# Kernel tuning notes

Hardware: AMD Instinct MI355X
Metric: run time of the kernel (lower is better)

## Reference

```python
import jax, jax.numpy as jnp
import numpy as np

# ---- constants from the source module ----
NB = [[0,1,2,3],[0,1,4],[0,2,5],[0,3,6],[1,4,7],[2,5,8],[3,6,9],[4,7,10],[5,8,11],[6,9],[7,10],[8,11],[12,13,14,15],[12,13,16],[12,14,17],[12,15],[13,16,18],[14,17,19],[16,18,20],[17,19,21],[18,20,22],[19,21,23],[20,22],[21,23]]
PARENT = np.array([0,0,0,0,1,2,3,4,5,6,7,8,9,9,9,12,13,14,16,17,18,19,20,21])  # root parent sentinel handled separately
KJ, NV, PREG = 24, 6890, 200
LEN = np.array([len(n) for n in NB])
NBR_IDX = np.zeros((KJ,4), np.int32)
NBR_VALID = np.zeros((KJ,4), np.float32)
for k, n in enumerate(NB):
    NBR_IDX[k,:len(n)] = n; NBR_VALID[k,:len(n)] = 1.0
BETA_POS = np.zeros((KJ,17), np.float32); BETA_POS[np.arange(KJ), 4*LEN] = 1.0
SLICE_MASK = np.zeros((23,17), np.float32)
for j in range(23):
    SLICE_MASK[j,:4*LEN[j]+1] = 1.0  # self.K[j] has 4*len(NB[j])+1 rows
NBR_IDX = jnp.asarray(NBR_IDX); NBR_VALID = jnp.asarray(NBR_VALID)
BETA_POS = jnp.asarray(BETA_POS); SLICE_MASK = jnpp = jnp.asarray(SLICE_MASK)


def setup_inputs() -> dict:
    key = jax.random.key(0)
    ks = jax.random.split(key, 9)
    V = jax.random.normal(ks[0], (PREG, NV, 3), jnp.float32)
    T = jax.random.normal(ks[1], (PREG, NV, 3), jnp.float32)
    J = jax.random.normal(ks[2], (PREG, KJ, 3), jnp.float32)
    theta = 0.3 * jax.random.normal(ks[3], (PREG, 72), jnp.float32)
    W_prime = jax.random.uniform(ks[4], (NV, KJ), jnp.float32)
    W_i = jax.random.uniform(ks[5], (NV, KJ), jnp.float32)
    W_i = W_i / W_i.sum(axis=1, keepdims=True)
    A = jax.random.uniform(ks[6], (23, NV), jnp.float32)
    K_mats = 0.01 * jax.random.normal(ks[7], (23, 17, 3 * NV), jnp.float32)
    K_mats = K_mats * SLICE_MASK[:, :, None]  # zero rows beyond the ragged per-joint size
    beta_2 = jnp.ones((1,), jnp.float32)
    return {"V": V, "T": T, "J": J, "theta": theta, "W_prime": W_prime, "W_i": W_i, "A": A, "K_mats": K_mats, "beta_2": beta_2, "epoch": 1}


def _rodrigues(pose):  # pose: (K,3)
    angle = jnp.maximum(jnp.linalg.norm(pose, axis=1, keepdims=True), 1e-8)
    axis = pose / angle
    x, y, z = axis[:, 0], axis[:, 1], axis[:, 2]
    zero = jnp.zeros_like(x)
    skew = jnp.stack([zero, -z, y, z, zero, -x, -y, x, zero], axis=1).reshape(-1, 3, 3)
    outer = axis[:, :, None] * axis[:, None, :]
    c = jnp.cos(angle)[:, :, None]
    s = jnp.sin(angle)[:, :, None]
    eye = jnp.eye(3, dtype=pose.dtype)[None]
    return c * eye + (1.0 - c) * outer + s * skew


def _compute_G(pose72, Jp):  # pose72: (72,), Jp: (K,3) -> (K,4,4)
    R = _rodrigues(pose72.reshape(KJ, 3))
    t = Jp - jnp.concatenate([jnp.zeros((1, 3), Jp.dtype), Jp[PARENT[1:]]], axis=0)
    G_local = jnp.zeros((KJ, 4, 4), Jp.dtype)
    G_local = G_local.at[:, :3, :3].set(R).at[:, :3, 3].set(t).at[:, 3, 3].set(1.0)
    Gs = [G_local[0]]
    for i in range(1, KJ):  # fixed 24-joint kinematic tree
        Gs.append(Gs[PARENT[i]] @ G_local[i])
    G = jnp.stack(Gs, axis=0)
    off = jnp.einsum('kij,kj->ki', G[:, :3, :3], Jp)  # homogeneous w=0 -> rotation only
    return G.at[:, :3, 3].add(-off)


def _axis2quat(p):  # (M,3) -> (M,4)
    angle = jnp.sqrt(jnp.maximum(jnp.sum(p ** 2, axis=1), 1e-16))
    n = p / angle[:, None]
    s = jnp.sin(angle / 2)
    return jnp.stack([n[:, 0] * s, n[:, 1] * s, n[:, 2] * s, jnp.cos(angle / 2) - 1.0], axis=1)


def reference(V, T, J, theta, W_prime, W_i, A, K_mats, beta_2, epoch):
    P = V.shape[0]
    b2 = beta_2[0]
    # normalized skinning weights
    W_relu = jax.nn.relu(W_prime)
    W_change = W_relu / (W_relu.sum(axis=1, keepdims=True) + 1e-8)
    # per-pose global joint transforms
    G_prime = jax.vmap(_compute_G)(theta, J)  # (P,K,4,4)
    # quaternion features and blend-shape correction
    q = _axis2quat(theta.reshape(P * KJ, 3)).reshape(P, KJ, 4)
    qg = q[:, NBR_IDX, :] * NBR_VALID[None, :, :, None]       # (P,K,4,4) neighbor gather
    q17 = jnp.concatenate([qg.reshape(P, KJ, 16), jnp.zeros((P, KJ, 1), q.dtype)], axis=-1)
    q17 = q17 + BETA_POS[None] * b2                            # beta_2 at column 4*len
    qm = q17[:, 1:, :] * SLICE_MASK[None]                      # ragged slice q_ne[:, j+1, :lenK]
    contrib = jnp.einsum('pjl,jlm->pjm', qm, K_mats).reshape(P, 23, NV, 3)
    T_p = jnp.einsum('pjnc,jn->pnc', contrib, jax.nn.relu(A)) + T
    # linear blend skinning
    T_h = jnp.concatenate([T_p, jnp.ones((P, NV, 1), T_p.dtype)], axis=-1)
    transformed = jnp.einsum('pkij,pnj->pnki', G_prime[:, :, :3, :], T_h)  # (P,N,K,3)
    verts = jnp.einsum('nk,pnkc->pnc', W_change, transformed)
    # energies
    e = float(epoch)
    g_wi = 0.1 * np.exp(-0.1 * e)
    g_w = 0.002 * np.exp(-0.008 * e)
    g_a = 0.001 * np.exp(-0.008 * e)
    g_k = 0.1 * np.exp(-0.008 * e)
    E_D = jnp.sum((V - verts) ** 2)
    E_Wi = jnp.sum((W_change - W_i) ** 2)
    E_W = jnp.sum(jnp.abs(W_change))
    E_A = jnp.sum(jnp.abs(A))
    E_K = jnp.sum(jnp.sqrt(jnp.sum(K_mats ** 2, axis=(1, 2))))
    E = E_D + g_wi * E_Wi + g_w * E_W + g_a * E_A + g_k * E_K
    return (E, verts)
```

## Files before the change

kernel.cpp:

```cpp
#include <hip/hip_runtime.h>
#include <math.h>

#define KJ 24
#define NV 6890
#define PREG 200
#define M_TOT (NV*3)
#define KDIM 391
#define KPAD 416
#define TP_STRIDE 20672
#define NMTILE 323

#define EDP_OFF 0
#define EKP_OFF 2816
#define WIP_OFF 10248
#define EWP_OFF 10280
#define EAP_OFF 10312
#define RED_OFF 10344
#define G_OFF   10384
#define WT_OFF  67984
#define RA_OFF  233344
#define QBH_OFF_U 1417600
#define QBL_OFF_U 1524096
#define TP_OFF  815296

typedef __attribute__((ext_vector_type(8))) short short8;
typedef __attribute__((ext_vector_type(4))) float f32x4;

__constant__ int c_PARENT[24] = {0,0,0,0,1,2,3,4,5,6,7,8,9,9,9,12,13,14,16,17,18,19,20,21};
__constant__ int c_DEPTH[24]  = {0,1,1,1,2,2,2,3,3,3,4,4,4,4,4,5,5,5,6,6,7,7,8,8};
__constant__ int c_LEN[24]    = {4,3,3,3,3,3,3,3,3,2,2,2,4,3,3,2,3,3,3,3,3,3,2,2};
__constant__ int c_NBR[24][4] = {
  {0,1,2,3},{0,1,4,0},{0,2,5,0},{0,3,6,0},{1,4,7,0},{2,5,8,0},{3,6,9,0},{4,7,10,0},
  {5,8,11,0},{6,9,0,0},{7,10,0,0},{8,11,0,0},{12,13,14,15},{12,13,16,0},{12,14,17,0},
  {12,15,0,0},{13,16,18,0},{14,17,19,0},{16,18,20,0},{17,19,21,0},{18,20,22,0},
  {19,21,23,0},{20,22,0,0},{21,23,0,0}};

__device__ __forceinline__ float waveReduce(float v) {
  #pragma unroll
  for (int off = 32; off > 0; off >>= 1) v += __shfl_down(v, off, 64);
  return v;
}
__device__ __forceinline__ unsigned short f2bf(float x) {
  union { float f; unsigned u; } v; v.f = x;
  unsigned r = v.u + 0x7FFFu + ((v.u >> 16) & 1u);
  return (unsigned short)(r >> 16);
}
__device__ __forceinline__ float bf2f(unsigned short h) {
  union { unsigned u; float f; } v; v.u = ((unsigned)h) << 16; return v.f;
}

__global__ __launch_bounds__(256) void kPre(const float* __restrict__ J,
                                            const float* __restrict__ theta,
                                            const float* __restrict__ beta2,
                                            const float* __restrict__ Wp,
                                            const float* __restrict__ Wi,
                                            const float* __restrict__ A,
                                            float* __restrict__ ws) {
  unsigned short* qbh = (unsigned short*)ws + QBH_OFF_U;
  unsigned short* qbl = (unsigned short*)ws + QBL_OFF_U;
  int b = blockIdx.x;
  if (b < 50) {
    __shared__ float Gl[4][24][12];
    __shared__ float Gg[4][24][12];
    __shared__ float q[4][24][4];
    int w = threadIdx.x >> 6, t = threadIdx.x & 63;
    int p = b*4 + w;
    if (t < 24) {
      float x = theta[p*72 + 3*t + 0];
      float y = theta[p*72 + 3*t + 1];
      float z = theta[p*72 + 3*t + 2];
      float n2 = x*x + y*y + z*z;
      float ang = fmaxf(sqrtf(n2), 1e-8f);
      float ia = 1.f/ang;
      float ax = x*ia, ay = y*ia, az = z*ia;
      float c = cosf(ang), s = sinf(ang), C = 1.f - c;
      float jx = J[p*72+3*t], jy = J[p*72+3*t+1], jz = J[p*72+3*t+2];
      float tx = jx, ty = jy, tz = jz;
      if (t > 0) {
        int par = c_PARENT[t];
        tx -= J[p*72+3*par]; ty -= J[p*72+3*par+1]; tz -= J[p*72+3*par+2];
      }
      Gl[w][t][0]=c+C*ax*ax;   Gl[w][t][1]=C*ax*ay-s*az; Gl[w][t][2]=C*ax*az+s*ay; Gl[w][t][3]=tx;
      Gl[w][t][4]=C*ax*ay+s*az;Gl[w][t][5]=c+C*ay*ay;    Gl[w][t][6]=C*ay*az-s*ax; Gl[w][t][7]=ty;
      Gl[w][t][8]=C*ax*az-s*ay;Gl[w][t][9]=C*ay*az+s*ax; Gl[w][t][10]=c+C*az*az;   Gl[w][t][11]=tz;
      float ang2 = sqrtf(fmaxf(n2, 1e-16f));
      float inv2 = 1.f/ang2;
      float s2 = sinf(0.5f*ang2);
      q[w][t][0] = x*inv2*s2; q[w][t][1] = y*inv2*s2; q[w][t][2] = z*inv2*s2;
      q[w][t][3] = cosf(0.5f*ang2) - 1.f;
    }
    __syncthreads();
    for (int lev = 0; lev <= 8; lev++) {
      if (t < 24 && c_DEPTH[t] == lev) {
        if (lev == 0) {
          for (int i2 = 0; i2 < 12; i2++) Gg[w][0][i2] = Gl[w][0][i2];
        } else {
          int par = c_PARENT[t];
          for (int r = 0; r < 3; r++) {
            float g0 = Gg[w][par][r*4+0], g1 = Gg[w][par][r*4+1];
            float g2 = Gg[w][par][r*4+2], g3 = Gg[w][par][r*4+3];
            for (int c2 = 0; c2 < 4; c2++) {
              float v = g0*Gl[w][t][0+c2] + g1*Gl[w][t][4+c2] + g2*Gl[w][t][8+c2];
              if (c2 == 3) v += g3;
              Gg[w][t][r*4+c2] = v;
            }
          }
        }
      }
      __syncthreads();
    }
    if (t < 24) {
      float jx = J[p*72+3*t], jy = J[p*72+3*t+1], jz = J[p*72+3*t+2];
      float* gp = ws + G_OFF + p*288 + t*12;
      #pragma unroll
      for (int r = 0; r < 3; r++) {
        float off = Gg[w][t][r*4+0]*jx + Gg[w][t][r*4+1]*jy + Gg[w][t][r*4+2]*jz;
        Gg[w][t][r*4+3] -= off;
      }
      #pragma unroll
      for (int i2 = 0; i2 < 12; i2++) gp[i2] = Gg[w][t][i2];
    }
    __syncthreads();
    float b2 = beta2[0];
    for (int e = t; e < KDIM; e += 64) {
      int j = e / 17, l = e - 17*j;
      int k = j + 1;
      float val = 0.f;
      if (l < 4*c_LEN[j] + 1) {
        if (l < 16) {
          int sidx = l >> 2, cc = l & 3;
          if (sidx < c_LEN[k]) val = q[w][c_NBR[k][sidx]][cc];
        }
        if (l == 4*c_LEN[k]) val += b2;
      }
      unsigned short hi = f2bf(val);
      unsigned short lo = f2bf(val - bf2f(hi));
      qbh[p*KPAD + e] = hi;
      qbl[p*KPAD + e] = lo;
    }
    for (int e = KDIM + t; e < KPAD; e += 64) {
      qbh[p*KPAD + e] = 0; qbl[p*KPAD + e] = 0;
    }
  } else {
    int d = b - 50;
    int t = threadIdx.x;
    int n = d*256 + t;
    float ewi = 0.f, ew = 0.f, ea = 0.f;
    if (n < NV) {
      float wv[24]; float sum = 0.f;
      const float4* wp4 = (const float4*)(Wp + n*24);
      #pragma unroll
      for (int i = 0; i < 6; i++) {
        float4 v4 = wp4[i];
        wv[4*i+0] = fmaxf(v4.x, 0.f); wv[4*i+1] = fmaxf(v4.y, 0.f);
        wv[4*i+2] = fmaxf(v4.z, 0.f); wv[4*i+3] = fmaxf(v4.w, 0.f);
        sum += wv[4*i+0]+wv[4*i+1]+wv[4*i+2]+wv[4*i+3];
      }
      float inv = 1.f/(sum + 1e-8f);
      #pragma unroll
      for (int k = 0; k < 24; k++) {
        float wc = wv[k]*inv;
        ws[WT_OFF + k*NV + n] = wc;
        ew += fabsf(wc);
        float dd = wc - Wi[n*24+k];
        ewi += dd*dd;
      }
    }
    for (int i = d*256 + t; i < 23*NV; i += 27*256) ea += fabsf(A[i]);
    for (int i = d*256 + t; i < 23*TP_STRIDE; i += 27*256) {
      int j = i / TP_STRIDE, m = i - j*TP_STRIDE;
      float v = 0.f;
      if (m < M_TOT) v = fmaxf(A[j*NV + m/3], 0.f);
      ws[RA_OFF + i] = v;
    }
    for (int i = d*256 + t; i < 56*KPAD; i += 27*256) {
      qbh[200*KPAD + i] = 0; qbl[200*KPAD + i] = 0;
    }
    __shared__ float red[3][4];
    int lane = t & 63, wv2 = t >> 6;
    ewi = waveReduce(ewi); ew = waveReduce(ew); ea = waveReduce(ea);
    if (lane == 0) { red[0][wv2] = ewi; red[1][wv2] = ew; red[2][wv2] = ea; }
    __syncthreads();
    if (t == 0) {
      ws[WIP_OFF + d] = red[0][0]+red[0][1]+red[0][2]+red[0][3];
      ws[EWP_OFF + d] = red[1][0]+red[1][1]+red[1][2]+red[1][3];
      ws[EAP_OFF + d] = red[2][0]+red[2][1]+red[2][2]+red[2][3];
    }
  }
}

__global__ __launch_bounds__(256, 2) void kB(const float* __restrict__ K,
                                             float* __restrict__ ws) {
  __shared__ unsigned short Bh[64*40];
  __shared__ unsigned short Bl[64*40];
  __shared__ float ek[23];
  const unsigned short* qbh = (const unsigned short*)ws + QBH_OFF_U;
  const unsigned short* qbl = (const unsigned short*)ws + QBL_OFF_U;
  float* __restrict__ TP = ws + TP_OFF;

  const int tid = threadIdx.x;
  const int bx = blockIdx.x;
  const int m0 = bx * 64;
  const int w = tid >> 6, lane = tid & 63;
  const int r = lane & 15, qd = lane >> 4;
  const int c4 = tid & 15, pr = tid >> 4;

  if (tid < 23) ek[tid] = 0.f;

  f32x4 acc[4][4];
  #pragma unroll
  for (int h = 0; h < 4; h++)
    #pragma unroll
    for (int f = 0; f < 4; f++) acc[h][f] = (f32x4){0.f,0.f,0.f,0.f};

  int aoff[4];
  #pragma unroll
  for (int h = 0; h < 4; h++) aoff[h] = (w*64 + h*16 + r) * KPAD + qd * 8;

  float wa[4], wb[4], sq0, sq1; int kg0, kg1;

  auto load_stage = [&](int ks) {
    int mm = m0 + 4*c4;
    kg0 = ks*32 + 2*pr; kg1 = kg0 + 1;
    float ka[4] = {0,0,0,0}, kc[4] = {0,0,0,0};
    sq0 = 0.f; sq1 = 0.f;
    #pragma unroll
    for (int i = 0; i < 4; i++) { wa[i] = 0.f; wb[i] = 0.f; }
    if (kg0 < KDIM) {
      int j = kg0 / 17;
      const float* kr = K + (size_t)kg0*M_TOT + mm;
      if (mm + 3 < M_TOT) {
        float2 x = *(const float2*)kr; float2 y = *(const float2*)(kr+2);
        ka[0]=x.x; ka[1]=x.y; ka[2]=y.x; ka[3]=y.y;
      } else {
        #pragma unroll
        for (int i = 0; i < 4; i++) if (mm+i < M_TOT) ka[i] = kr[i];
      }
      float4 ra = *(const float4*)(ws + RA_OFF + (size_t)j*TP_STRIDE + mm);
      wa[0]=ka[0]*ra.x; wa[1]=ka[1]*ra.y; wa[2]=ka[2]*ra.z; wa[3]=ka[3]*ra.w;
      sq0 = ka[0]*ka[0]+ka[1]*ka[1]+ka[2]*ka[2]+ka[3]*ka[3];
    }
    if (kg1 < KDIM) {
      int j = kg1 / 17;
      const float* kr = K + (size_t)kg1*M_TOT + mm;
      if (mm + 3 < M_TOT) {
        float2 x = *(const float2*)kr; float2 y = *(const float2*)(kr+2);
        kc[0]=x.x; kc[1]=x.y; kc[2]=y.x; kc[3]=y.y;
      } else {
        #pragma unroll
        for (int i = 0; i < 4; i++) if (mm+i < M_TOT) kc[i] = kr[i];
      }
      float4 ra = *(const float4*)(ws + RA_OFF + (size_t)j*TP_STRIDE + mm);
      wb[0]=kc[0]*ra.x; wb[1]=kc[1]*ra.y; wb[2]=kc[2]*ra.z; wb[3]=kc[3]*ra.w;
      sq1 = kc[0]*kc[0]+kc[1]*kc[1]+kc[2]*kc[2]+kc[3]*kc[3];
    }
  };
  auto write_stage = [&]() {
    #pragma unroll
    for (int i = 0; i < 4; i++) {
      unsigned short h0 = f2bf(wa[i]); unsigned short l0 = f2bf(wa[i] - bf2f(h0));
      unsigned short h1 = f2bf(wb[i]); unsigned short l1 = f2bf(wb[i] - bf2f(h1));
      int mi = 4*c4 + i;
      *(unsigned*)&Bh[mi*40 + pr*2] = (unsigned)h0 | ((unsigned)h1 << 16);
      *(unsigned*)&Bl[mi*40 + pr*2] = (unsigned)l0 | ((unsigned)l1 << 16);
    }
    #pragma unroll
    for (int off = 1; off <= 8; off <<= 1) {
      sq0 += __shfl_xor(sq0, off, 64);
      sq1 += __shfl_xor(sq1, off, 64);
    }
    if ((lane & 15) == 0) {
      if (kg0 < KDIM) atomicAdd(&ek[kg0/17], sq0);
      if (kg1 < KDIM) atomicAdd(&ek[kg1/17], sq1);
    }
  };

  load_stage(0);
  for (int ks = 0; ks < 13; ks++) {
    __syncthreads();
    write_stage();
    if (ks + 1 < 13) load_stage(ks + 1);
    __syncthreads();
    int kso = ks * 32;
    short8 ah[4], al[4];
    #pragma unroll
    for (int h = 0; h < 4; h++) {
      ah[h] = *(const short8*)(qbh + aoff[h] + kso);
      al[h] = *(const short8*)(qbl + aoff[h] + kso);
    }
    #pragma unroll
    for (int f = 0; f < 4; f++) {
      int m = f*16 + r;
      short8 bh = *(const short8*)(&Bh[m*40 + qd*8]);
      short8 bl = *(const short8*)(&Bl[m*40 + qd*8]);
      #pragma unroll
      for (int h = 0; h < 4; h++) {
        acc[h][f] = __builtin_amdgcn_mfma_f32_16x16x32_bf16(ah[h], bh, acc[h][f], 0, 0, 0);
        acc[h][f] = __builtin_amdgcn_mfma_f32_16x16x32_bf16(ah[h], bl, acc[h][f], 0, 0, 0);
        acc[h][f] = __builtin_amdgcn_mfma_f32_16x16x32_bf16(al[h], bh, acc[h][f], 0, 0, 0);
      }
    }
  }
  #pragma unroll
  for (int h = 0; h < 4; h++)
    #pragma unroll
    for (int f = 0; f < 4; f++)
      #pragma unroll
      for (int g = 0; g < 4; g++) {
        int p = w*64 + h*16 + qd*4 + g;
        TP[(size_t)p*TP_STRIDE + m0 + f*16 + r] = acc[h][f][g];
      }
  __syncthreads();
  if (tid < 23)
    ws[EKP_OFF + tid*NMTILE + bx] = ek[tid];
}

__global__ __launch_bounds__(256) void kC(const float* __restrict__ V,
                                          const float* __restrict__ T,
                                          float* __restrict__ ws,
                                          float* __restrict__ out) {
  int p = blockIdx.y;
  int n0 = (blockIdx.x*256 + threadIdx.x) * 2;
  __shared__ float Gs[288];
  __shared__ float tmp[4];
  if (threadIdx.x < 72)
    ((float4*)Gs)[threadIdx.x] = ((const float4*)(ws + G_OFF + p*288))[threadIdx.x];
  __syncthreads();
  float ed = 0.f;
  if (n0 < NV) {
    float M0[12], M1[12];
    #pragma unroll
    for (int i = 0; i < 12; i++) { M0[i] = 0.f; M1[i] = 0.f; }
    const float* Wt = ws + WT_OFF;
    #pragma unroll
    for (int k = 0; k < 24; k++) {
      float2 wv = *(const float2*)(Wt + k*NV + n0);
      float4 g0 = *(const float4*)(Gs + k*12 + 0);
      float4 g1 = *(const float4*)(Gs + k*12 + 4);
      float4 g2 = *(const float4*)(Gs + k*12 + 8);
      M0[0] = fmaf(wv.x, g0.x, M0[0]); M0[1]  = fmaf(wv.x, g0.y, M0[1]);
      M0[2] = fmaf(wv.x, g0.z, M0[2]); M0[3]  = fmaf(wv.x, g0.w, M0[3]);
      M0[4] = fmaf(wv.x, g1.x, M0[4]); M0[5]  = fmaf(wv.x, g1.y, M0[5]);
      M0[6] = fmaf(wv.x, g1.z, M0[6]); M0[7]  = fmaf(wv.x, g1.w, M0[7]);
      M0[8] = fmaf(wv.x, g2.x, M0[8]); M0[9]  = fmaf(wv.x, g2.y, M0[9]);
      M0[10]= fmaf(wv.x, g2.z, M0[10]);M0[11] = fmaf(wv.x, g2.w, M0[11]);
      M1[0] = fmaf(wv.y, g0.x, M1[0]); M1[1]  = fmaf(wv.y, g0.y, M1[1]);
      M1[2] = fmaf(wv.y, g0.z, M1[2]); M1[3]  = fmaf(wv.y, g0.w, M1[3]);
      M1[4] = fmaf(wv.y, g1.x, M1[4]); M1[5]  = fmaf(wv.y, g1.y, M1[5]);
      M1[6] = fmaf(wv.y, g1.z, M1[6]); M1[7]  = fmaf(wv.y, g1.w, M1[7]);
      M1[8] = fmaf(wv.y, g2.x, M1[8]); M1[9]  = fmaf(wv.y, g2.y, M1[9]);
      M1[10]= fmaf(wv.y, g2.z, M1[10]);M1[11] = fmaf(wv.y, g2.w, M1[11]);
    }
    size_t tb = (size_t)p*M_TOT + 3*n0;
    size_t pb = (size_t)p*TP_STRIDE + 3*n0;
    float2 q0 = *(const float2*)(ws + TP_OFF + pb);
    float2 q1 = *(const float2*)(ws + TP_OFF + pb + 2);
    float2 q2 = *(const float2*)(ws + TP_OFF + pb + 4);
    float2 s0 = *(const float2*)(T + tb);
    float2 s1 = *(const float2*)(T + tb + 2);
    float2 s2 = *(const float2*)(T + tb + 4);
    float ta0 = q0.x + s0.x, ta1 = q0.y + s0.y, ta2 = q1.x + s1.x;
    float tb0 = q1.y + s1.y, tb1 = q2.x + s2.x, tb2 = q2.y + s2.y;
    float v00 = M0[0]*ta0 + M0[1]*ta1 + M0[2]*ta2  + M0[3];
    float v01 = M0[4]*ta0 + M0[5]*ta1 + M0[6]*ta2  + M0[7];
    float v02 = M0[8]*ta0 + M0[9]*ta1 + M0[10]*ta2 + M0[11];
    float v10 = M1[0]*tb0 + M1[1]*tb1 + M1[2]*tb2  + M1[3];
    float v11 = M1[4]*tb0 + M1[5]*tb1 + M1[6]*tb2  + M1[7];
    float v12 = M1[8]*tb0 + M1[9]*tb1 + M1[10]*tb2 + M1[11];
    out[1+tb+0] = v00; out[1+tb+1] = v01; out[1+tb+2] = v02;
    out[1+tb+3] = v10; out[1+tb+4] = v11; out[1+tb+5] = v12;
    float2 x0 = *(const float2*)(V + tb);
    float2 x1 = *(const float2*)(V + tb + 2);
    float2 x2 = *(const float2*)(V + tb + 4);
    float d0 = x0.x-v00, d1 = x0.y-v01, d2 = x1.x-v02;
    float d3 = x1.y-v10, d4 = x2.x-v11, d5 = x2.y-v12;
    ed = d0*d0 + d1*d1 + d2*d2 + d3*d3 + d4*d4 + d5*d5;
  }
  ed = waveReduce(ed);
  int lane = threadIdx.x & 63, w = threadIdx.x >> 6;
  if (lane == 0) tmp[w] = ed;
  __syncthreads();
  if (threadIdx.x == 0)
    ws[EDP_OFF + blockIdx.y*14 + blockIdx.x] = tmp[0]+tmp[1]+tmp[2]+tmp[3];
}

__global__ __launch_bounds__(256) void kF1(float* __restrict__ ws) {
  __shared__ float sb[4];
  int b = blockIdx.x, t = threadIdx.x, lane = t & 63, w = t >> 6;
  if (b < 23) {
    float s = 0.f;
    for (int i = t; i < NMTILE; i += 256) s += ws[EKP_OFF + b*NMTILE + i];
    s = waveReduce(s);
    if (lane == 0) sb[w] = s;
    __syncthreads();
    if (t == 0) ws[RED_OFF + b] = sb[0]+sb[1]+sb[2]+sb[3];
  } else if (b == 23) {
    float s = 0.f;
    for (int i = t; i < 2800; i += 256) s += ws[EDP_OFF + i];
    s = waveReduce(s);
    if (lane == 0) sb[w] = s;
    __syncthreads();
    if (t == 0) ws[RED_OFF + 23] = sb[0]+sb[1]+sb[2]+sb[3];
  } else {
    if (w == 0) {
      float s = (lane < 27) ? ws[WIP_OFF + lane] : 0.f;
      s = waveReduce(s);
      if (lane == 0) ws[RED_OFF + 24] = s;
    } else if (w == 1) {
      float s = (lane < 27) ? ws[EWP_OFF + lane] : 0.f;
      s = waveReduce(s);
      if (lane == 0) ws[RED_OFF + 25] = s;
    } else if (w == 2) {
      float s = (lane < 27) ? ws[EAP_OFF + lane] : 0.f;
      s = waveReduce(s);
      if (lane == 0) ws[RED_OFF + 26] = s;
    }
  }
}

__global__ void kF2(const int* __restrict__ epoch, const float* __restrict__ ws,
                    float* __restrict__ out) {
  int t = threadIdx.x;
  float s = (t < 23) ? sqrtf(ws[RED_OFF + t]) : 0.f;
  s = waveReduce(s);
  if (t == 0) {
    float e    = (float)epoch[0];
    float g_wi = 0.1f   * expf(-0.1f  * e);
    float g_w  = 0.002f * expf(-0.008f* e);
    float g_a  = 0.001f * expf(-0.008f* e);
    float g_k  = 0.1f   * expf(-0.008f* e);
    out[0] = ws[RED_OFF+23] + g_wi*ws[RED_OFF+24] + g_w*ws[RED_OFF+25]
           + g_a*ws[RED_OFF+26] + g_k*s;
  }
}

extern "C" void kernel_launch(void* const* d_in, const int* in_sizes, int n_in,
                              void* d_out, int out_size, void* d_ws, size_t ws_size,
                              hipStream_t stream) {
  const float* V     = (const float*)d_in[0];
  const float* T     = (const float*)d_in[1];
  const float* J     = (const float*)d_in[2];
  const float* theta = (const float*)d_in[3];
  const float* Wp    = (const float*)d_in[4];
  const float* Wi    = (const float*)d_in[5];
  const float* A     = (const float*)d_in[6];
  const float* K     = (const float*)d_in[7];
  const float* b2    = (const float*)d_in[8];
  const int*   epoch = (const int*)d_in[9];
  float* out = (float*)d_out;
  float* ws  = (float*)d_ws;

  hipLaunchKernelGGL(kPre, dim3(77),       dim3(256), 0, stream,
                     J, theta, b2, Wp, Wi, A, ws);
  hipLaunchKernelGGL(kB,   dim3(NMTILE),   dim3(256), 0, stream, K, ws);
  hipLaunchKernelGGL(kC,   dim3(14, PREG), dim3(256), 0, stream, V, T, ws, out);
  hipLaunchKernelGGL(kF1,  dim3(25),       dim3(256), 0, stream, ws);
  hipLaunchKernelGGL(kF2,  dim3(1),        dim3(64),  0, stream, epoch, ws, out);
}
```

Measured before the change: 207.4 us.

## Precompute bf16 hi/lo transposed weighted K in prologue, stream B from global in GEMM

The K*relu(A) weighting and its bf16 hi/lo split move out of the GEMM kernel into extra blocks of the prologue kernel. These blocks write a transposed, K-contiguous B matrix to the workspace. The GEMM then loads B fragments straight from global with register double-buffering, uses a 32-wide M tile across twice as many blocks, and drops its LDS staging and barriers. The skinning kernel now recomputes the normalized weights from W_prime per vertex, at one vertex per thread, instead of reading a stored transposed weight array. The cost is an extra global round trip for the split B matrix (about 17 MB written and then read back) and more partial sums to reduce.

```diff
diff --git a/kernel.cpp b/kernel.cpp
--- a/kernel.cpp
+++ b/kernel.cpp
@@ -8,23 +8,26 @@
 #define KDIM 391
 #define KPAD 416
 #define TP_STRIDE 20672
-#define NMTILE 323
+#define NMT64 323
+#define NSTAGE (NMT64*13)
+#define NMT32 646
 
 #define EDP_OFF 0
-#define EKP_OFF 2816
-#define WIP_OFF 10248
-#define EWP_OFF 10280
-#define EAP_OFF 10312
-#define RED_OFF 10344
-#define G_OFF   10384
-#define WT_OFF  67984
-#define RA_OFF  233344
-#define QBH_OFF_U 1417600
-#define QBL_OFF_U 1524096
-#define TP_OFF  815296
+#define EKP_OFF 5400
+#define WIP_OFF 101984
+#define EWP_OFF 102016
+#define EAP_OFF 102048
+#define RED_OFF 102080
+#define G_OFF   102112
+#define TP_OFF  159712
+#define QBH_OFF_U 10903488
+#define QBL_OFF_U 11009984
+#define BTH_OFF_U 11116480
+#define BTL_OFF_U 19716032
 
 typedef __attribute__((ext_vector_type(8))) short short8;
 typedef __attribute__((ext_vector_type(4))) float f32x4;
+typedef __attribute__((ext_vector_type(4))) unsigned int u32x4;
 
 __constant__ int c_PARENT[24] = {0,0,0,0,1,2,3,4,5,6,7,8,9,9,9,12,13,14,16,17,18,19,20,21};
 __constant__ int c_DEPTH[24]  = {0,1,1,1,2,2,2,3,3,3,4,4,4,4,4,5,5,5,6,6,7,7,8,8};
@@ -55,6 +58,7 @@
                                             const float* __restrict__ Wp,
                                             const float* __restrict__ Wi,
                                             const float* __restrict__ A,
+                                            const float* __restrict__ K,
                                             float* __restrict__ ws) {
   unsigned short* qbh = (unsigned short*)ws + QBH_OFF_U;
   unsigned short* qbl = (unsigned short*)ws + QBL_OFF_U;
@@ -141,7 +145,7 @@
     for (int e = KDIM + t; e < KPAD; e += 64) {
       qbh[p*KPAD + e] = 0; qbl[p*KPAD + e] = 0;
     }
-  } else {
+  } else if (b < 77) {
     int d = b - 50;
     int t = threadIdx.x;
     int n = d*256 + t;
@@ -160,19 +164,12 @@
       #pragma unroll
       for (int k = 0; k < 24; k++) {
         float wc = wv[k]*inv;
-        ws[WT_OFF + k*NV + n] = wc;
         ew += fabsf(wc);
         float dd = wc - Wi[n*24+k];
         ewi += dd*dd;
       }
     }
     for (int i = d*256 + t; i < 23*NV; i += 27*256) ea += fabsf(A[i]);
-    for (int i = d*256 + t; i < 23*TP_STRIDE; i += 27*256) {
-      int j = i / TP_STRIDE, m = i - j*TP_STRIDE;
-      float v = 0.f;
-      if (m < M_TOT) v = fmaxf(A[j*NV + m/3], 0.f);
-      ws[RA_OFF + i] = v;
-    }
     for (int i = d*256 + t; i < 56*KPAD; i += 27*256) {
       qbh[200*KPAD + i] = 0; qbl[200*KPAD + i] = 0;
     }
@@ -186,202 +183,198 @@
       ws[EWP_OFF + d] = red[1][0]+red[1][1]+red[1][2]+red[1][3];
       ws[EAP_OFF + d] = red[2][0]+red[2][1]+red[2][2]+red[2][3];
     }
-  }
-}
-
-__global__ __launch_bounds__(256, 2) void kB(const float* __restrict__ K,
-                                             float* __restrict__ ws) {
-  __shared__ unsigned short Bh[64*40];
-  __shared__ unsigned short Bl[64*40];
-  __shared__ float ek[23];
+  } else {
+    int flat = b - 77;
+    int bx = flat % NMT64, by = flat / NMT64;
+    int m0 = bx*64, kg0 = by*32;
+    __shared__ unsigned short Sh[32*66];
+    __shared__ unsigned short Sl[32*66];
+    __shared__ float ek[23];
+    int t = threadIdx.x;
+    if (t < 23) ek[t] = 0.f;
+    __syncthreads();
+    int krow = t >> 3, mseg = (t & 7) * 8;
+    int kg = kg0 + krow;
+    int mm = m0 + mseg;
+    float kv[8], wv[8]; float sq = 0.f;
+    #pragma unroll
+    for (int i = 0; i < 8; i++) { kv[i] = 0.f; wv[i] = 0.f; }
+    if (kg < KDIM) {
+      const float* kr = K + (size_t)kg*M_TOT + mm;
+      if (mm + 7 < M_TOT) {
+        float4 a4 = *(const float4*)kr; float4 b4 = *(const float4*)(kr+4);
+        kv[0]=a4.x; kv[1]=a4.y; kv[2]=a4.z; kv[3]=a4.w;
+        kv[4]=b4.x; kv[5]=b4.y; kv[6]=b4.z; kv[7]=b4.w;
+      } else {
+        #pragma unroll
+        for (int i = 0; i < 8; i++) if (mm+i < M_TOT) kv[i] = kr[i];
+      }
+      int j = kg / 17;
+      #pragma unroll
+      for (int i = 0; i < 8; i++) {
+        float av = (mm+i < M_TOT) ? fmaxf(A[j*NV + (mm+i)/3], 0.f) : 0.f;
+        wv[i] = kv[i]*av;
+        sq = fmaf(kv[i], kv[i], sq);
+      }
+    }
+    #pragma unroll
+    for (int c = 0; c < 4; c++) {
+      unsigned short h0 = f2bf(wv[2*c]),  h1 = f2bf(wv[2*c+1]);
+      unsigned short l0 = f2bf(wv[2*c]   - bf2f(h0));
+      unsigned short l1 = f2bf(wv[2*c+1] - bf2f(h1));
+      *(unsigned*)&Sh[krow*66 + mseg + 2*c] = (unsigned)h0 | ((unsigned)h1 << 16);
+      *(unsigned*)&Sl[krow*66 + mseg + 2*c] = (unsigned)l0 | ((unsigned)l1 << 16);
+    }
+    sq += __shfl_xor(sq, 1, 64);
+    sq += __shfl_xor(sq, 2, 64);
+    sq += __shfl_xor(sq, 4, 64);
+    if ((t & 7) == 0 && kg < KDIM) atomicAdd(&ek[kg/17], sq);
+    __syncthreads();
+    int mrow = t >> 2, kq = t & 3;
+    unsigned dh[4], dl[4];
+    #pragma unroll
+    for (int c2 = 0; c2 < 4; c2++) {
+      unsigned short s0 = Sh[(kq*8 + 2*c2    )*66 + mrow];
+      unsigned short s1 = Sh[(kq*8 + 2*c2 + 1)*66 + mrow];
+      dh[c2] = (unsigned)s0 | ((unsigned)s1 << 16);
+      unsigned short u0 = Sl[(kq*8 + 2*c2    )*66 + mrow];
+      unsigned short u1 = Sl[(kq*8 + 2*c2 + 1)*66 + mrow];
+      dl[c2] = (unsigned)u0 | ((unsigned)u1 << 16);
+    }
+    unsigned short* BtH = (unsigned short*)ws + BTH_OFF_U;
+    unsigned short* BtL = (unsigned short*)ws + BTL_OFF_U;
+    size_t o = (size_t)(m0 + mrow)*KPAD + kg0 + kq*8;
+    *(u32x4*)(BtH + o) = (u32x4){dh[0], dh[1], dh[2], dh[3]};
+    *(u32x4*)(BtL + o) = (u32x4){dl[0], dl[1], dl[2], dl[3]};
+    if (t < 23) ws[EKP_OFF + t*NSTAGE + flat] = ek[t];
+  }
+}
+
+__global__ __launch_bounds__(256) void kB(float* __restrict__ ws) {
   const unsigned short* qbh = (const unsigned short*)ws + QBH_OFF_U;
   const unsigned short* qbl = (const unsigned short*)ws + QBL_OFF_U;
+  const unsigned short* BtH = (const unsigned short*)ws + BTH_OFF_U;
+  const unsigned short* BtL = (const unsigned short*)ws + BTL_OFF_U;
   float* __restrict__ TP = ws + TP_OFF;
-
-  const int tid = threadIdx.x;
-  const int bx = blockIdx.x;
-  const int m0 = bx * 64;
+  const int tid = threadIdx.x, bx = blockIdx.x;
+  const int m0 = bx * 32;
   const int w = tid >> 6, lane = tid & 63;
   const int r = lane & 15, qd = lane >> 4;
-  const int c4 = tid & 15, pr = tid >> 4;
-
-  if (tid < 23) ek[tid] = 0.f;
-
-  f32x4 acc[4][4];
+
+  f32x4 acc[4][2];
   #pragma unroll
   for (int h = 0; h < 4; h++)
     #pragma unroll
-    for (int f = 0; f < 4; f++) acc[h][f] = (f32x4){0.f,0.f,0.f,0.f};
-
-  int aoff[4];
-  #pragma unroll
-  for (int h = 0; h < 4; h++) aoff[h] = (w*64 + h*16 + r) * KPAD + qd * 8;
-
-  float wa[4], wb[4], sq0, sq1; int kg0, kg1;
-
-  auto load_stage = [&](int ks) {
-    int mm = m0 + 4*c4;
-    kg0 = ks*32 + 2*pr; kg1 = kg0 + 1;
-    float ka[4] = {0,0,0,0}, kc[4] = {0,0,0,0};
-    sq0 = 0.f; sq1 = 0.f;
-    #pragma unroll
-    for (int i = 0; i < 4; i++) { wa[i] = 0.f; wb[i] = 0.f; }
-    if (kg0 < KDIM) {
-      int j = kg0 / 17;
-      const float* kr = K + (size_t)kg0*M_TOT + mm;
-      if (mm + 3 < M_TOT) {
-        float2 x = *(const float2*)kr; float2 y = *(const float2*)(kr+2);
-        ka[0]=x.x; ka[1]=x.y; ka[2]=y.x; ka[3]=y.y;
-      } else {
-        #pragma unroll
-        for (int i = 0; i < 4; i++) if (mm+i < M_TOT) ka[i] = kr[i];
-      }
-      float4 ra = *(const float4*)(ws + RA_OFF + (size_t)j*TP_STRIDE + mm);
-      wa[0]=ka[0]*ra.x; wa[1]=ka[1]*ra.y; wa[2]=ka[2]*ra.z; wa[3]=ka[3]*ra.w;
-      sq0 = ka[0]*ka[0]+ka[1]*ka[1]+ka[2]*ka[2]+ka[3]*ka[3];
-    }
-    if (kg1 < KDIM) {
-      int j = kg1 / 17;
-      const float* kr = K + (size_t)kg1*M_TOT + mm;
-      if (mm + 3 < M_TOT) {
-        float2 x = *(const float2*)kr; float2 y = *(const float2*)(kr+2);
-        kc[0]=x.x; kc[1]=x.y; kc[2]=y.x; kc[3]=y.y;
-      } else {
-        #pragma unroll
-        for (int i = 0; i < 4; i++) if (mm+i < M_TOT) kc[i] = kr[i];
-      }
-      float4 ra = *(const float4*)(ws + RA_OFF + (size_t)j*TP_STRIDE + mm);
-      wb[0]=kc[0]*ra.x; wb[1]=kc[1]*ra.y; wb[2]=kc[2]*ra.z; wb[3]=kc[3]*ra.w;
-      sq1 = kc[0]*kc[0]+kc[1]*kc[1]+kc[2]*kc[2]+kc[3]*kc[3];
-    }
-  };
-  auto write_stage = [&]() {
-    #pragma unroll
-    for (int i = 0; i < 4; i++) {
-      unsigned short h0 = f2bf(wa[i]); unsigned short l0 = f2bf(wa[i] - bf2f(h0));
-      unsigned short h1 = f2bf(wb[i]); unsigned short l1 = f2bf(wb[i] - bf2f(h1));
-      int mi = 4*c4 + i;
-      *(unsigned*)&Bh[mi*40 + pr*2] = (unsigned)h0 | ((unsigned)h1 << 16);
-      *(unsigned*)&Bl[mi*40 + pr*2] = (unsigned)l0 | ((unsigned)l1 << 16);
-    }
-    #pragma unroll
-    for (int off = 1; off <= 8; off <<= 1) {
-      sq0 += __shfl_xor(sq0, off, 64);
-      sq1 += __shfl_xor(sq1, off, 64);
-    }
-    if ((lane & 15) == 0) {
-      if (kg0 < KDIM) atomicAdd(&ek[kg0/17], sq0);
-      if (kg1 < KDIM) atomicAdd(&ek[kg1/17], sq1);
-    }
-  };
-
-  load_stage(0);
+    for (int f = 0; f < 2; f++) acc[h][f] = (f32x4){0.f,0.f,0.f,0.f};
+
+  int aofs[4], bofs[2];
+  #pragma unroll
+  for (int h = 0; h < 4; h++) aofs[h] = (w*64 + h*16 + r)*KPAD + qd*8;
+  #pragma unroll
+  for (int f = 0; f < 2; f++) bofs[f] = (m0 + f*16 + r)*KPAD + qd*8;
+
+  short8 bh[2][2], bl[2][2];
+  #pragma unroll
+  for (int f = 0; f < 2; f++) {
+    bh[0][f] = *(const short8*)(BtH + bofs[f]);
+    bl[0][f] = *(const short8*)(BtL + bofs[f]);
+  }
+  #pragma unroll
   for (int ks = 0; ks < 13; ks++) {
-    __syncthreads();
-    write_stage();
-    if (ks + 1 < 13) load_stage(ks + 1);
-    __syncthreads();
-    int kso = ks * 32;
+    const int cur = ks & 1, nxt = cur ^ 1;
+    if (ks + 1 < 13) {
+      #pragma unroll
+      for (int f = 0; f < 2; f++) {
+        bh[nxt][f] = *(const short8*)(BtH + bofs[f] + (ks+1)*32);
+        bl[nxt][f] = *(const short8*)(BtL + bofs[f] + (ks+1)*32);
+      }
+    }
     short8 ah[4], al[4];
     #pragma unroll
     for (int h = 0; h < 4; h++) {
-      ah[h] = *(const short8*)(qbh + aoff[h] + kso);
-      al[h] = *(const short8*)(qbl + aoff[h] + kso);
-    }
-    #pragma unroll
-    for (int f = 0; f < 4; f++) {
-      int m = f*16 + r;
-      short8 bh = *(const short8*)(&Bh[m*40 + qd*8]);
-      short8 bl = *(const short8*)(&Bl[m*40 + qd*8]);
+      ah[h] = *(const short8*)(qbh + aofs[h] + ks*32);
+      al[h] = *(const short8*)(qbl + aofs[h] + ks*32);
+    }
+    #pragma unroll
+    for (int f = 0; f < 2; f++)
       #pragma unroll
       for (int h = 0; h < 4; h++) {
-        acc[h][f] = __builtin_amdgcn_mfma_f32_16x16x32_bf16(ah[h], bh, acc[h][f], 0, 0, 0);
-        acc[h][f] = __builtin_amdgcn_mfma_f32_16x16x32_bf16(ah[h], bl, acc[h][f], 0, 0, 0);
-        acc[h][f] = __builtin_amdgcn_mfma_f32_16x16x32_bf16(al[h], bh, acc[h][f], 0, 0, 0);
-      }
-    }
+        acc[h][f] = __builtin_amdgcn_mfma_f32_16x16x32_bf16(ah[h], bh[cur][f], acc[h][f], 0, 0, 0);
+        acc[h][f] = __builtin_amdgcn_mfma_f32_16x16x32_bf16(ah[h], bl[cur][f], acc[h][f], 0, 0, 0);
+        acc[h][f] = __builtin_amdgcn_mfma_f32_16x16x32_bf16(al[h], bh[cur][f], acc[h][f], 0, 0, 0);
+      }
   }
   #pragma unroll
   for (int h = 0; h < 4; h++)
     #pragma unroll
-    for (int f = 0; f < 4; f++)
+    for (int f = 0; f < 2; f++)
       #pragma unroll
       for (int g = 0; g < 4; g++) {
         int p = w*64 + h*16 + qd*4 + g;
         TP[(size_t)p*TP_STRIDE + m0 + f*16 + r] = acc[h][f][g];
       }
-  __syncthreads();
-  if (tid < 23)
-    ws[EKP_OFF + tid*NMTILE + bx] = ek[tid];
 }
 
 __global__ __launch_bounds__(256) void kC(const float* __restrict__ V,
                                           const float* __restrict__ T,
+                                          const float* __restrict__ Wp,
                                           float* __restrict__ ws,
                                           float* __restrict__ out) {
   int p = blockIdx.y;
-  int n0 = (blockIdx.x*256 + threadIdx.x) * 2;
+  int n = blockIdx.x*256 + threadIdx.x;
   __shared__ float Gs[288];
   __shared__ float tmp[4];
   if (threadIdx.x < 72)
     ((float4*)Gs)[threadIdx.x] = ((const float4*)(ws + G_OFF + p*288))[threadIdx.x];
   __syncthreads();
   float ed = 0.f;
-  if (n0 < NV) {
-    float M0[12], M1[12];
-    #pragma unroll
-    for (int i = 0; i < 12; i++) { M0[i] = 0.f; M1[i] = 0.f; }
-    const float* Wt = ws + WT_OFF;
+  if (n < NV) {
+    float wv[24]; float sum = 0.f;
+    const float4* wp4 = (const float4*)(Wp + n*24);
+    #pragma unroll
+    for (int i = 0; i < 6; i++) {
+      float4 v4 = wp4[i];
+      wv[4*i+0] = fmaxf(v4.x, 0.f); wv[4*i+1] = fmaxf(v4.y, 0.f);
+      wv[4*i+2] = fmaxf(v4.z, 0.f); wv[4*i+3] = fmaxf(v4.w, 0.f);
+      sum += wv[4*i+0]+wv[4*i+1]+wv[4*i+2]+wv[4*i+3];
+    }
+    float inv = 1.f/(sum + 1e-8f);
+    float M[12];
+    #pragma unroll
+    for (int i = 0; i < 12; i++) M[i] = 0.f;
     #pragma unroll
     for (int k = 0; k < 24; k++) {
-      float2 wv = *(const float2*)(Wt + k*NV + n0);
+      float wc = wv[k];
       float4 g0 = *(const float4*)(Gs + k*12 + 0);
       float4 g1 = *(const float4*)(Gs + k*12 + 4);
       float4 g2 = *(const float4*)(Gs + k*12 + 8);
-      M0[0] = fmaf(wv.x, g0.x, M0[0]); M0[1]  = fmaf(wv.x, g0.y, M0[1]);
-      M0[2] = fmaf(wv.x, g0.z, M0[2]); M0[3]  = fmaf(wv.x, g0.w, M0[3]);
-      M0[4] = fmaf(wv.x, g1.x, M0[4]); M0[5]  = fmaf(wv.x, g1.y, M0[5]);
-      M0[6] = fmaf(wv.x, g1.z, M0[6]); M0[7]  = fmaf(wv.x, g1.w, M0[7]);
-      M0[8] = fmaf(wv.x, g2.x, M0[8]); M0[9]  = fmaf(wv.x, g2.y, M0[9]);
-      M0[10]= fmaf(wv.x, g2.z, M0[10]);M0[11] = fmaf(wv.x, g2.w, M0[11]);
-      M1[0] = fmaf(wv.y, g0.x, M1[0]); M1[1]  = fmaf(wv.y, g0.y, M1[1]);
-      M1[2] = fmaf(wv.y, g0.z, M1[2]); M1[3]  = fmaf(wv.y, g0.w, M1[3]);
-      M1[4] = fmaf(wv.y, g1.x, M1[4]); M1[5]  = fmaf(wv.y, g1.y, M1[5]);
-      M1[6] = fmaf(wv.y, g1.z, M1[6]); M1[7]  = fmaf(wv.y, g1.w, M1[7]);
-      M1[8] = fmaf(wv.y, g2.x, M1[8]); M1[9]  = fmaf(wv.y, g2.y, M1[9]);
-      M1[10]= fmaf(wv.y, g2.z, M1[10]);M1[11] = fmaf(wv.y, g2.w, M1[11]);
-    }
-    size_t tb = (size_t)p*M_TOT + 3*n0;
-    size_t pb = (size_t)p*TP_STRIDE + 3*n0;
-    float2 q0 = *(const float2*)(ws + TP_OFF + pb);
-    float2 q1 = *(const float2*)(ws + TP_OFF + pb + 2);
-    float2 q2 = *(const float2*)(ws + TP_OFF + pb + 4);
-    float2 s0 = *(const float2*)(T + tb);
-    float2 s1 = *(const float2*)(T + tb + 2);
-    float2 s2 = *(const float2*)(T + tb + 4);
-    float ta0 = q0.x + s0.x, ta1 = q0.y + s0.y, ta2 = q1.x + s1.x;
-    float tb0 = q1.y + s1.y, tb1 = q2.x + s2.x, tb2 = q2.y + s2.y;
-    float v00 = M0[0]*ta0 + M0[1]*ta1 + M0[2]*ta2  + M0[3];
-    float v01 = M0[4]*ta0 + M0[5]*ta1 + M0[6]*ta2  + M0[7];
-    float v02 = M0[8]*ta0 + M0[9]*ta1 + M0[10]*ta2 + M0[11];
-    float v10 = M1[0]*tb0 + M1[1]*tb1 + M1[2]*tb2  + M1[3];
-    float v11 = M1[4]*tb0 + M1[5]*tb1 + M1[6]*tb2  + M1[7];
-    float v12 = M1[8]*tb0 + M1[9]*tb1 + M1[10]*tb2 + M1[11];
-    out[1+tb+0] = v00; out[1+tb+1] = v01; out[1+tb+2] = v02;
-    out[1+tb+3] = v10; out[1+tb+4] = v11; out[1+tb+5] = v12;
-    float2 x0 = *(const float2*)(V + tb);
-    float2 x1 = *(const float2*)(V + tb + 2);
-    float2 x2 = *(const float2*)(V + tb + 4);
-    float d0 = x0.x-v00, d1 = x0.y-v01, d2 = x1.x-v02;
-    float d3 = x1.y-v10, d4 = x2.x-v11, d5 = x2.y-v12;
-    ed = d0*d0 + d1*d1 + d2*d2 + d3*d3 + d4*d4 + d5*d5;
+      M[0] = fmaf(wc, g0.x, M[0]); M[1]  = fmaf(wc, g0.y, M[1]);
+      M[2] = fmaf(wc, g0.z, M[2]); M[3]  = fmaf(wc, g0.w, M[3]);
+      M[4] = fmaf(wc, g1.x, M[4]); M[5]  = fmaf(wc, g1.y, M[5]);
+      M[6] = fmaf(wc, g1.z, M[6]); M[7]  = fmaf(wc, g1.w, M[7]);
+      M[8] = fmaf(wc, g2.x, M[8]); M[9]  = fmaf(wc, g2.y, M[9]);
+      M[10]= fmaf(wc, g2.z, M[10]);M[11] = fmaf(wc, g2.w, M[11]);
+    }
+    #pragma unroll
+    for (int i = 0; i < 12; i++) M[i] *= inv;
+    size_t tb = (size_t)p*M_TOT + 3*n;
+    size_t pb = (size_t)p*TP_STRIDE + 3*n;
+    float t0 = ws[TP_OFF + pb + 0] + T[tb + 0];
+    float t1 = ws[TP_OFF + pb + 1] + T[tb + 1];
+    float t2 = ws[TP_OFF + pb + 2] + T[tb + 2];
+    float v0 = M[0]*t0 + M[1]*t1 + M[2]*t2  + M[3];
+    float v1 = M[4]*t0 + M[5]*t1 + M[6]*t2  + M[7];
+    float v2 = M[8]*t0 + M[9]*t1 + M[10]*t2 + M[11];
+    out[1+tb+0] = v0; out[1+tb+1] = v1; out[1+tb+2] = v2;
+    float d0 = V[tb+0]-v0, d1 = V[tb+1]-v1, d2 = V[tb+2]-v2;
+    ed = d0*d0 + d1*d1 + d2*d2;
   }
   ed = waveReduce(ed);
   int lane = threadIdx.x & 63, w = threadIdx.x >> 6;
   if (lane == 0) tmp[w] = ed;
   __syncthreads();
   if (threadIdx.x == 0)
-    ws[EDP_OFF + blockIdx.y*14 + blockIdx.x] = tmp[0]+tmp[1]+tmp[2]+tmp[3];
+    ws[EDP_OFF + blockIdx.y*27 + blockIdx.x] = tmp[0]+tmp[1]+tmp[2]+tmp[3];
 }
 
 __global__ __launch_bounds__(256) void kF1(float* __restrict__ ws) {
@@ -389,14 +382,14 @@
   int b = blockIdx.x, t = threadIdx.x, lane = t & 63, w = t >> 6;
   if (b < 23) {
     float s = 0.f;
-    for (int i = t; i < NMTILE; i += 256) s += ws[EKP_OFF + b*NMTILE + i];
+    for (int i = t; i < NSTAGE; i += 256) s += ws[EKP_OFF + b*NSTAGE + i];
     s = waveReduce(s);
     if (lane == 0) sb[w] = s;
     __syncthreads();
     if (t == 0) ws[RED_OFF + b] = sb[0]+sb[1]+sb[2]+sb[3];
   } else if (b == 23) {
     float s = 0.f;
-    for (int i = t; i < 2800; i += 256) s += ws[EDP_OFF + i];
+    for (int i = t; i < 5400; i += 256) s += ws[EDP_OFF + i];
     s = waveReduce(s);
     if (lane == 0) sb[w] = s;
     __syncthreads();
@@ -450,10 +443,10 @@
   float* out = (float*)d_out;
   float* ws  = (float*)d_ws;
 
-  hipLaunchKernelGGL(kPre, dim3(77),       dim3(256), 0, stream,
-                     J, theta, b2, Wp, Wi, A, ws);
-  hipLaunchKernelGGL(kB,   dim3(NMTILE),   dim3(256), 0, stream, K, ws);
-  hipLaunchKernelGGL(kC,   dim3(14, PREG), dim3(256), 0, stream, V, T, ws, out);
-  hipLaunchKernelGGL(kF1,  dim3(25),       dim3(256), 0, stream, ws);
-  hipLaunchKernelGGL(kF2,  dim3(1),        dim3(64),  0, stream, epoch, ws, out);
-}
+  hipLaunchKernelGGL(kPre, dim3(77 + NSTAGE), dim3(256), 0, stream,
+                     J, theta, b2, Wp, Wi, A, K, ws);
+  hipLaunchKernelGGL(kB,   dim3(NMT32),       dim3(256), 0, stream, ws);
+  hipLaunchKernelGGL(kC,   dim3(27, PREG),    dim3(256), 0, stream, V, T, Wp, ws, out);
+  hipLaunchKernelGGL(kF1,  dim3(25),          dim3(256), 0, stream, ws);
+  hipLaunchKernelGGL(kF2,  dim3(1),           dim3(64),  0, stream, epoch, ws, out);
+}
```

Result: faster. 201.9 us (-2.6%).
